# Kernel optimization log

Hardware: AMD Instinct MI355X
Metric: run time of the kernel (lower is better)

## Reference

```python
import jax, jax.numpy as jnp
import numpy as np

N_NODES = 100000
N_EDGES = 1600000
N_GRAPHS = 128


def _gru(x, w_ih, w_hh, b_ih, b_hh):
    # x: [N, T, D]; torch nn.GRU single layer, batch_first
    N, T, D = x.shape
    H = w_hh.shape[1]
    gi = jnp.einsum('ntd,gd->ntg', x, w_ih) + b_ih  # [N, T, 3H]

    def step(h, g_t):
        gh = h @ w_hh.T + b_hh
        i_r, i_z, i_n = jnp.split(g_t, 3, axis=-1)
        h_r, h_z, h_n = jnp.split(gh, 3, axis=-1)
        r = jax.nn.sigmoid(i_r + h_r)
        z = jax.nn.sigmoid(i_z + h_z)
        n = jnp.tanh(i_n + r * h_n)
        h_new = (1 - z) * n + z * h
        return h_new, None

    h0 = jnp.zeros((N, H), x.dtype)
    h, _ = jax.lax.scan(step, h0, jnp.swapaxes(gi, 0, 1))
    return h  # [N, H]


def _gat(x, W, att_src, att_dst, bias, src, dst, num_nodes, concat):
    # PyG GATConv: linear, per-head attention logits, segment softmax over dst, scatter-add
    H, C = att_src.shape
    xs = (x @ W).reshape(num_nodes, H, C)
    a_src = (xs * att_src).sum(-1)  # [N, H]
    a_dst = (xs * att_dst).sum(-1)  # [N, H]
    e = jax.nn.leaky_relu(a_src[src] + a_dst[dst], 0.2)  # [E, H]
    emax = jax.ops.segment_max(e, dst, num_segments=num_nodes)
    ee = jnp.exp(e - emax[dst])
    denom = jax.ops.segment_sum(ee, dst, num_segments=num_nodes)
    alpha = ee / (denom[dst] + 1e-16)
    msg = xs[src] * alpha[:, :, None]  # [E, H, C]
    out = jax.ops.segment_sum(msg, dst, num_segments=num_nodes)  # [N, H, C]
    if concat:
        out = out.reshape(num_nodes, H * C)
    else:
        out = out.mean(axis=1)
    return out + bias


def setup_inputs() -> dict:
    key = jax.random.key(0)
    ks = jax.random.split(key, 20)
    s = 0.05
    inp = {
        'x': jax.random.normal(ks[0], (N_NODES, 8, 128), jnp.float32),
        'edge_index': jax.random.randint(ks[1], (2, N_EDGES), 0, N_NODES, jnp.int32),
        'batch': jnp.sort(jax.random.randint(ks[2], (N_NODES,), 0, N_GRAPHS, jnp.int32)),
        'num_graphs': N_GRAPHS,
        'gru_w_ih': jax.random.normal(ks[3], (192, 128)) * s,
        'gru_w_hh': jax.random.normal(ks[4], (192, 64)) * s,
        'gru_b_ih': jax.random.normal(ks[5], (192,)) * s,
        'gru_b_hh': jax.random.normal(ks[6], (192,)) * s,
        'W1': jax.random.normal(ks[7], (64, 256)) * s,
        'att_src1': jax.random.normal(ks[8], (4, 64)) * s,
        'att_dst1': jax.random.normal(ks[9], (4, 64)) * s,
        'b1': jax.random.normal(ks[10], (256,)) * s,
        'W2': jax.random.normal(ks[11], (256, 64)) * s,
        'att_src2': jax.random.normal(ks[12], (1, 64)) * s,
        'att_dst2': jax.random.normal(ks[13], (1, 64)) * s,
        'b2': jax.random.normal(ks[14], (64,)) * s,
        'attn_w': jax.random.normal(ks[15], (64, 1)) * s,
        'attn_b': jax.random.normal(ks[16], (1,)) * s,
        'fc_w': jax.random.normal(ks[17], (64, 10)) * s,
        'fc_b': jax.random.normal(ks[18], (10,)) * s,
    }
    return inp


def reference(x, edge_index, batch, num_graphs, gru_w_ih, gru_w_hh, gru_b_ih, gru_b_hh,
              W1, att_src1, att_dst1, b1, W2, att_src2, att_dst2, b2,
              attn_w, attn_b, fc_w, fc_b):
    N = x.shape[0]
    h = _gru(x, gru_w_ih, gru_w_hh, gru_b_ih, gru_b_hh)  # [N, 64]
    # GATConv default add_self_loops=True
    loops = jnp.arange(N, dtype=edge_index.dtype)
    src = jnp.concatenate([edge_index[0], loops])
    dst = jnp.concatenate([edge_index[1], loops])
    h = jax.nn.relu(_gat(h, W1, att_src1, att_dst1, b1, src, dst, N, concat=True))   # [N, 256]
    h = jax.nn.relu(_gat(h, W2, att_src2, att_dst2, b2, src, dst, N, concat=False))  # [N, 64]
    # softmax over dim=1 of [N,1] -> all ones (faithful to the original code)
    aw = jax.nn.softmax(h @ attn_w + attn_b, axis=1)  # [N, 1]
    weighted = aw * h
    sums = jax.ops.segment_sum(weighted, batch, num_segments=num_graphs)  # [G, 64]
    counts = jax.ops.segment_sum(jnp.ones((N,), h.dtype), batch, num_segments=num_graphs)
    graph_feat = sums / jnp.maximum(counts, 1.0)[:, None]
    out = graph_feat @ fc_w + fc_b
    return jax.nn.log_softmax(out, axis=-1)
```

## Files before the change

kernel.cpp:

```cpp
#include <hip/hip_runtime.h>
#include <stdint.h>


typedef __attribute__((ext_vector_type(8))) short short8;
typedef __attribute__((ext_vector_type(4))) float f32x4;
typedef __attribute__((ext_vector_type(2))) float f32x2;
typedef __attribute__((ext_vector_type(2))) unsigned int u32x2;
typedef __attribute__((ext_vector_type(4))) unsigned int u32x4;

__device__ __forceinline__ unsigned short f2bf(float f) {
    unsigned u = __float_as_uint(f);
    u += 0x7FFFu + ((u >> 16) & 1u);
    return (unsigned short)(u >> 16);
}
__device__ __forceinline__ unsigned cvtpk(float lo, float hi) {
    unsigned r;
    asm("v_cvt_pk_bf16_f32 %0, %1, %2" : "=v"(r) : "v"(lo), "v"(hi));
    return r;
}
__device__ __forceinline__ unsigned short f2bfq(float v) {
    unsigned r;
    asm("v_cvt_pk_bf16_f32 %0, %1, %1" : "=v"(r) : "v"(v));
    return (unsigned short)r;
}
__device__ __forceinline__ float lrelu(float x) { return x > 0.f ? x : 0.2f * x; }
__device__ __forceinline__ float fsig(float a) {
    return __builtin_amdgcn_rcpf(1.f + __expf(-a));
}
__device__ __forceinline__ float ftanh(float a) {
    return 2.f * __builtin_amdgcn_rcpf(1.f + __expf(-2.f * a)) - 1.f;
}
__device__ __forceinline__ unsigned enc4fp8(float a, float b, float c, float d) {
    unsigned r = __builtin_amdgcn_cvt_pk_fp8_f32(a, b, 0, false);
    r = __builtin_amdgcn_cvt_pk_fp8_f32(c, d, r, true);
    return r;
}
__device__ __forceinline__ unsigned char enc1fp8(float v) {
    return (unsigned char)(__builtin_amdgcn_cvt_pk_fp8_f32(v, v, 0, false) & 0xff);
}

__device__ void pack_body(const float* __restrict__ src, unsigned short* __restrict__ dst,
                          int K, int NCOL, int ldsrc, int transposed, int blk, int tid) {
    int id = blk * 256 + tid;
    int KT = K >> 5;
    int nfrag = (NCOL >> 4) * KT;
    if (id >= nfrag * 64) return;
    int l = id & 63;
    int f = id >> 6;
    int kt = f % KT, ct = f / KT;
    int col = ct * 16 + (l & 15);
    int kbase = kt * 32 + ((l >> 4) << 3);
#pragma unroll
    for (int i = 0; i < 8; i++) {
        int k = kbase + i;
        float v = transposed ? src[(size_t)col * ldsrc + k] : src[(size_t)k * ldsrc + col];
        dst[((size_t)f * 64 + l) * 8 + i] = f2bf(v);
    }
}
__device__ void packv_body(const float* __restrict__ W, const float* __restrict__ avs,
                           const float* __restrict__ avd, unsigned short* __restrict__ dst,
                           int K, int H, int ldW, int blk, int tid) {
    int id = blk * 256 + tid;
    int KT = K >> 5;
    if (id >= KT * 64) return;
    int l = id & 63, f = id >> 6;
    int col = l & 15;
    int kbase = f * 32 + ((l >> 4) << 3);
    for (int i = 0; i < 8; i++) {
        int k = kbase + i;
        float val = 0.f;
        if (col < 2 * H) {
            int h = col >> 1;
            const float* av = (col & 1) ? avd : avs;
            for (int c = 0; c < 64; c++) val += W[(size_t)k * ldW + h * 64 + c] * av[h * 64 + c];
        }
        dst[((size_t)f * 64 + l) * 8 + i] = f2bf(val);
    }
}
__global__ void k_prep(const float* w_ih, const float* w_hh, const float* W1, const float* W2,
                       const float* as1, const float* ad1, const float* as2, const float* ad2,
                       const float* b1,
                       unsigned short* p_gi, unsigned short* p_gh,
                       unsigned short* p_w1, unsigned short* p_w2,
                       unsigned short* p_v1, unsigned short* p_v2,
                       float* b1p, int* cursor, int N) {
    int b = blockIdx.x, tid = threadIdx.x;
    if (b >= 38) {
        int i = (b - 38) * 256 + tid;
        if (i < N) cursor[i] = 0;
        return;
    }
    if (b < 12)      pack_body(w_ih, p_gi, 128, 192, 128, 1, b, tid);
    else if (b < 18) pack_body(w_hh, p_gh, 64, 192, 64, 1, b - 12, tid);
    else if (b < 26) pack_body(W1, p_w1, 64, 256, 256, 0, b - 18, tid);
    else if (b < 34) pack_body(W2, p_w2, 256, 64, 64, 0, b - 26, tid);
    else if (b < 35) packv_body(W1, as1, ad1, p_v1, 64, 4, 256, b - 34, tid);
    else if (b < 37) packv_body(W2, as2, ad2, p_v2, 256, 1, 64, b - 35, tid);
    else {
        int o = tid;
        int p = (o & 0xC0) | ((o & 15) << 2) | ((o >> 4) & 3);
        b1p[p] = b1[o];
    }
}

__launch_bounds__(256, 2)
__global__ void k_gru_gemm1(const float* __restrict__ x,
                            const unsigned short* __restrict__ pgi,
                            const unsigned short* __restrict__ pgh,
                            const float* __restrict__ b_ih, const float* __restrict__ b_hh,
                            const unsigned short* __restrict__ packB,
                            const unsigned short* __restrict__ pv1,
                            unsigned char* __restrict__ Cf,
                            float* __restrict__ aS, float* __restrict__ aD, int N) {
    __shared__ unsigned short x_pack[4 * 4 * 64 * 8];
    __shared__ unsigned short h_pack[4 * 2 * 64 * 8];

    const int tid = threadIdx.x;
    const int w = tid >> 6;
    const int l = tid & 63;
    const int row0 = blockIdx.x * 64;

    short8 wgi[3][4], wgh[3][2];
#pragma unroll
    for (int g = 0; g < 3; g++) {
        int ctg = g * 4 + w;
#pragma unroll
        for (int kt = 0; kt < 4; kt++)
            wgi[g][kt] = *(const short8*)(pgi + ((size_t)(ctg * 4 + kt) * 64 + l) * 8);
#pragma unroll
        for (int kt = 0; kt < 2; kt++)
            wgh[g][kt] = *(const short8*)(pgh + ((size_t)(ctg * 2 + kt) * 64 + l) * 8);
    }
    const int j = (w << 4) + (l & 15);
    const float bs_r = b_ih[j] + b_hh[j];
    const float bs_z = b_ih[64 + j] + b_hh[64 + j];
    const float bi_n = b_ih[128 + j], bh_n = b_hh[128 + j];

    f32x4 hreg[4];
    const f32x4 z4 = {0.f, 0.f, 0.f, 0.f};
#pragma unroll
    for (int m = 0; m < 4; m++) hreg[m] = z4;

    const int sr = tid >> 2, sub = tid & 3;
    const int snode = min(row0 + sr, N - 1);
    const int slane = (sr & 15) | (sub << 4);
    const int sm = sr >> 4;
    const float* xbase = x + (size_t)snode * 1024;

    float4 pre[8];
#pragma unroll
    for (int it = 0; it < 4; it++) {
        int d0 = it * 32 + sub * 8;
        pre[2 * it] = *(const float4*)(xbase + d0);
        pre[2 * it + 1] = *(const float4*)(xbase + d0 + 4);
    }

    for (int t = 0; t < 8; t++) {
        u32x4 pk[4];
#pragma unroll
        for (int it = 0; it < 4; it++) {
            float4 va = pre[2 * it], vb = pre[2 * it + 1];
            u32x4 p;
            p[0] = cvtpk(va.x, va.y); p[1] = cvtpk(va.z, va.w);
            p[2] = cvtpk(vb.x, vb.y); p[3] = cvtpk(vb.z, vb.w);
            pk[it] = p;
        }
        if (t > 0) {
#pragma unroll
            for (int m = 0; m < 4; m++)
#pragma unroll
                for (int q = 0; q < 4; q++) {
                    int rl = ((l >> 4) << 2) + q;
                    int lane2 = rl | (((j >> 3) & 3) << 4);
                    h_pack[((m * 2 + (j >> 5)) * 64 + lane2) * 8 + (j & 7)] = f2bfq(hreg[m][q]);
                }
        }
#pragma unroll
        for (int it = 0; it < 4; it++)
            *(u32x4*)&x_pack[((sm * 4 + it) * 64 + slane) * 8] = pk[it];
        __syncthreads();

        if (t < 7) {
            const float* xp = xbase + (t + 1) * 128;
#pragma unroll
            for (int it = 0; it < 4; it++) {
                int d0 = it * 32 + sub * 8;
                pre[2 * it] = *(const float4*)(xp + d0);
                pre[2 * it + 1] = *(const float4*)(xp + d0 + 4);
            }
        }

        f32x4 agi[4][3], aghn[4];
#pragma unroll
        for (int m = 0; m < 4; m++) {
            agi[m][0] = z4; agi[m][1] = z4; agi[m][2] = z4; aghn[m] = z4;
        }

#pragma unroll
        for (int m = 0; m < 4; m++) {
#pragma unroll
            for (int kt = 0; kt < 4; kt++) {
                short8 a = *(const short8*)&x_pack[((m * 4 + kt) * 64 + l) * 8];
#pragma unroll
                for (int g = 0; g < 3; g++)
                    agi[m][g] = __builtin_amdgcn_mfma_f32_16x16x32_bf16(a, wgi[g][kt], agi[m][g], 0, 0, 0);
            }
            if (t > 0) {
#pragma unroll
                for (int kt = 0; kt < 2; kt++) {
                    short8 a = *(const short8*)&h_pack[((m * 2 + kt) * 64 + l) * 8];
                    agi[m][0] = __builtin_amdgcn_mfma_f32_16x16x32_bf16(a, wgh[0][kt], agi[m][0], 0, 0, 0);
                    agi[m][1] = __builtin_amdgcn_mfma_f32_16x16x32_bf16(a, wgh[1][kt], agi[m][1], 0, 0, 0);
                    aghn[m]   = __builtin_amdgcn_mfma_f32_16x16x32_bf16(a, wgh[2][kt], aghn[m], 0, 0, 0);
                }
            }
        }
#pragma unroll
        for (int m = 0; m < 4; m++) {
#pragma unroll
            for (int q = 0; q < 4; q++) {
                float rr = fsig(agi[m][0][q] + bs_r);
                float zz = fsig(agi[m][1][q] + bs_z);
                float hn = aghn[m][q] + bh_n;
                float nn = ftanh(agi[m][2][q] + bi_n + rr * hn);
                hreg[m][q] = nn + zz * (hreg[m][q] - nn);
            }
        }
        __syncthreads();
    }

    short8 bfw[4][2];
#pragma unroll
    for (int ci = 0; ci < 4; ci++)
#pragma unroll
        for (int kt = 0; kt < 2; kt++)
            bfw[ci][kt] = *(const short8*)(packB + ((size_t)((w * 4 + ci) * 2 + kt) * 64 + l) * 8);
    short8 bev[2];
#pragma unroll
    for (int kt = 0; kt < 2; kt++)
        bev[kt] = *(const short8*)(pv1 + ((size_t)kt * 64 + l) * 8);

#pragma unroll
    for (int m = 0; m < 4; m++)
#pragma unroll
        for (int q = 0; q < 4; q++) {
            int rl = ((l >> 4) << 2) + q;
            int lane2 = rl | (((j >> 3) & 3) << 4);
            h_pack[((m * 2 + (j >> 5)) * 64 + lane2) * 8 + (j & 7)] = f2bfq(hreg[m][q]);
        }
    __syncthreads();

    f32x4 acc[4][4];
#pragma unroll
    for (int m = 0; m < 4; m++)
#pragma unroll
        for (int ci = 0; ci < 4; ci++) acc[m][ci] = z4;

#pragma unroll
    for (int m = 0; m < 4; m++)
#pragma unroll
        for (int kt = 0; kt < 2; kt++) {
            short8 a = *(const short8*)&h_pack[((m * 2 + kt) * 64 + l) * 8];
#pragma unroll
            for (int ci = 0; ci < 4; ci++)
                acc[m][ci] = __builtin_amdgcn_mfma_f32_16x16x32_bf16(a, bfw[ci][kt], acc[m][ci], 0, 0, 0);
        }

    f32x4 acce = z4;
#pragma unroll
    for (int kt = 0; kt < 2; kt++) {
        short8 a = *(const short8*)&h_pack[((w * 2 + kt) * 64 + l) * 8];
        acce = __builtin_amdgcn_mfma_f32_16x16x32_bf16(a, bev[kt], acce, 0, 0, 0);
    }
    int colE = l & 15;
    if (colE < 8) {
        int h = colE >> 1;
#pragma unroll
        for (int q = 0; q < 4; q++) {
            int node = row0 + (w << 4) + ((l >> 4) << 2) + q;
            if (node < N) {
                if (colE & 1) aD[node * 4 + h] = acce[q];
                else          aS[node * 4 + h] = acce[q];
            }
        }
    }
    const int lc = l & 15;
#pragma unroll
    for (int m = 0; m < 4; m++)
#pragma unroll
        for (int q = 0; q < 4; q++) {
            int node = row0 + (m << 4) + ((l >> 4) << 2) + q;
            if (node < N) {
                unsigned d = enc4fp8(acc[m][0][q], acc[m][1][q], acc[m][2][q], acc[m][3][q]);
                *(unsigned*)(Cf + (size_t)node * 256 + w * 64 + lc * 4) = d;
            }
        }
}

__global__ void k_fill(const int* __restrict__ srcv, const int* __restrict__ dstv,
                       int* __restrict__ cursor, int* __restrict__ ssrc, int E) {
    int i = blockIdx.x * blockDim.x + threadIdx.x;
    if (i < E) {
        int d = dstv[i];
        int pos = atomicAdd(&cursor[d], 1);
        if (pos < 64) ssrc[(size_t)d * 64 + pos] = srcv[i];
    }
}

__global__ void k_agg1(const unsigned char* __restrict__ xs,
                       const float* __restrict__ a_s, const float* __restrict__ a_d,
                       const int* __restrict__ deg, const int* __restrict__ ssrc,
                       const float* __restrict__ b1p,
                       unsigned short* __restrict__ h2, int N) {
    const int v = blockIdx.x * 16 + (threadIdx.x >> 4);
    if (v >= N) return;
    const int cq = threadIdx.x & 15;
    const int H = cq >> 2;
    const float adv = a_d[v * 4 + H];
    const int cnt = min(deg[v], 64);
    const size_t base = (size_t)v * 64;

    float s_;
    float ac[16];
    {
        u32x4 xv = *(const u32x4*)(xs + (size_t)v * 256 + cq * 16);
        float pv = __expf(lrelu(a_s[v * 4 + H] + adv));
        s_ = pv;
#pragma unroll
        for (int wd = 0; wd < 4; wd++) {
            f32x2 lo = __builtin_amdgcn_cvt_pk_f32_fp8(xv[wd], false);
            f32x2 hi = __builtin_amdgcn_cvt_pk_f32_fp8(xv[wd], true);
            ac[wd * 4 + 0] = pv * lo[0]; ac[wd * 4 + 1] = pv * lo[1];
            ac[wd * 4 + 2] = pv * hi[0]; ac[wd * 4 + 3] = pv * hi[1];
        }
    }

#define AG1_LOAD(S, POS) { int pp = min((POS), cl); int uu = ssrc[base + pp]; \
        aa##S = a_s[uu * 4 + H]; x##S = *(const u32x4*)(xs + (size_t)uu * 256 + cq * 16); }
#define AG1_PROC(S, PRED) { float p = (PRED) ? __expf(lrelu(aa##S + adv)) : 0.f; s_ += p; \
        _Pragma("unroll") for (int wd = 0; wd < 4; wd++) { \
            f32x2 lo = __builtin_amdgcn_cvt_pk_f32_fp8(x##S[wd], false); \
            f32x2 hi = __builtin_amdgcn_cvt_pk_f32_fp8(x##S[wd], true); \
            ac[wd * 4 + 0] += p * lo[0]; ac[wd * 4 + 1] += p * lo[1]; \
            ac[wd * 4 + 2] += p * hi[0]; ac[wd * 4 + 3] += p * hi[1]; } }

    float aa0 = 0.f, aa1 = 0.f, aa2 = 0.f, aa3 = 0.f;
    u32x4 x0 = {0,0,0,0}, x1 = {0,0,0,0}, x2 = {0,0,0,0}, x3 = {0,0,0,0};
    if (cnt > 0) {
        const int cl = cnt - 1;
        AG1_LOAD(0, 0) AG1_LOAD(1, 1) AG1_LOAD(2, 2) AG1_LOAD(3, 3)
        int k = 0;
        for (; k + 4 <= cnt; k += 4) {
            AG1_PROC(0, true) AG1_LOAD(0, k + 4)
            AG1_PROC(1, true) AG1_LOAD(1, k + 5)
            AG1_PROC(2, true) AG1_LOAD(2, k + 6)
            AG1_PROC(3, true) AG1_LOAD(3, k + 7)
        }
        AG1_PROC(0, k + 0 < cnt)
        AG1_PROC(1, k + 1 < cnt)
        AG1_PROC(2, k + 2 < cnt)
        AG1_PROC(3, k + 3 < cnt)
    }
#undef AG1_LOAD
#undef AG1_PROC

    float inv = __builtin_amdgcn_rcpf(s_ + 1e-16f);
    float bp[16];
#pragma unroll
    for (int i = 0; i < 4; i++)
        *(float4*)&bp[i * 4] = *(const float4*)(b1p + cq * 16 + i * 4);
#pragma unroll
    for (int b = 0; b < 4; b++) {
        float r0 = fmaxf(ac[b]      * inv + bp[b],      0.f);
        float r1 = fmaxf(ac[4 + b]  * inv + bp[4 + b],  0.f);
        float r2 = fmaxf(ac[8 + b]  * inv + bp[8 + b],  0.f);
        float r3 = fmaxf(ac[12 + b] * inv + bp[12 + b], 0.f);
        u32x2 o;
        o[0] = cvtpk(r0, r1); o[1] = cvtpk(r2, r3);
        *(u32x2*)(h2 + (size_t)v * 256 + H * 64 + b * 16 + (cq & 3) * 4) = o;
    }
}

__launch_bounds__(256, 2)
__global__ void k_gemm2(const unsigned short* __restrict__ A,
                        const unsigned short* __restrict__ packB,
                        const unsigned short* __restrict__ pv2,
                        unsigned char* __restrict__ Cf,
                        float* __restrict__ aS, float* __restrict__ aD, int N) {
    constexpr int KT = 8;
    __shared__ unsigned short a_pack[4 * KT * 64 * 8];

    const int tid = threadIdx.x, w = tid >> 6, l = tid & 63;
    const int row0 = blockIdx.x * 64;

    short8 bf[KT];
#pragma unroll
    for (int kt = 0; kt < KT; kt++)
        bf[kt] = *(const short8*)(packB + ((size_t)(w * KT + kt) * 64 + l) * 8);

    const int sr = tid >> 2, sub = tid & 3;
    const int snode = min(row0 + sr, N - 1);
    const unsigned short* ap = A + (size_t)snode * 256;
#pragma unroll
    for (int it = 0; it < KT; it++) {
        int d0 = it * 32 + sub * 8;
        short8 v = *(const short8*)(ap + d0);
        *(short8*)&a_pack[(((sr >> 4) * KT + it) * 64 + ((sr & 15) | (sub << 4))) * 8] = v;
    }
    __syncthreads();

    const f32x4 z4 = {0.f, 0.f, 0.f, 0.f};
    f32x4 acc[4];
#pragma unroll
    for (int m = 0; m < 4; m++) acc[m] = z4;

#pragma unroll
    for (int m = 0; m < 4; m++)
#pragma unroll
        for (int kt = 0; kt < KT; kt++) {
            short8 a = *(const short8*)&a_pack[((m * KT + kt) * 64 + l) * 8];
            acc[m] = __builtin_amdgcn_mfma_f32_16x16x32_bf16(a, bf[kt], acc[m], 0, 0, 0);
        }

    f32x4 acce = z4;
#pragma unroll
    for (int kt = 0; kt < KT; kt++) {
        short8 be = *(const short8*)(pv2 + ((size_t)kt * 64 + l) * 8);
        short8 a = *(const short8*)&a_pack[((w * KT + kt) * 64 + l) * 8];
        acce = __builtin_amdgcn_mfma_f32_16x16x32_bf16(a, be, acce, 0, 0, 0);
    }
    int colE = l & 15;
    if (colE < 2) {
#pragma unroll
        for (int q = 0; q < 4; q++) {
            int node = row0 + (w << 4) + ((l >> 4) << 2) + q;
            if (node < N) {
                if (colE) aD[node] = acce[q];
                else      aS[node] = acce[q];
            }
        }
    }

    int colw = w * 16 + (l & 15);
#pragma unroll
    for (int m = 0; m < 4; m++)
#pragma unroll
        for (int q = 0; q < 4; q++) {
            int node = row0 + (m << 4) + ((l >> 4) << 2) + q;
            if (node < N) Cf[(size_t)node * 64 + colw] = enc1fp8(acc[m][q]);
        }
}

__global__ void k_agg2(const unsigned char* __restrict__ xs,
                       const float* __restrict__ a_s, const float* __restrict__ a_d,
                       const int* __restrict__ deg, const int* __restrict__ ssrc,
                       const float* __restrict__ bias,
                       float* __restrict__ out, int N) {
    const int v = blockIdx.x * 32 + (threadIdx.x >> 3);
    if (v >= N) return;
    const int cq = threadIdx.x & 7;
    const int c0 = cq * 8;
    const float adv = a_d[v];
    const int cnt = min(deg[v], 64);
    const size_t base = (size_t)v * 64;

    float s_;
    float ac[8];
    {
        u32x2 xv = *(const u32x2*)(xs + (size_t)v * 64 + c0);
        float pv = __expf(lrelu(a_s[v] + adv));
        s_ = pv;
#pragma unroll
        for (int wd = 0; wd < 2; wd++) {
            f32x2 lo = __builtin_amdgcn_cvt_pk_f32_fp8(xv[wd], false);
            f32x2 hi = __builtin_amdgcn_cvt_pk_f32_fp8(xv[wd], true);
            ac[wd * 4 + 0] = pv * lo[0]; ac[wd * 4 + 1] = pv * lo[1];
            ac[wd * 4 + 2] = pv * hi[0]; ac[wd * 4 + 3] = pv * hi[1];
        }
    }

#define AG2_LOAD(S, POS) { int pp = min((POS), cl); int uu = ssrc[base + pp]; \
        aa##S = a_s[uu]; x##S = *(const u32x2*)(xs + (size_t)uu * 64 + c0); }
#define AG2_PROC(S, PRED) { float p = (PRED) ? __expf(lrelu(aa##S + adv)) : 0.f; s_ += p; \
        _Pragma("unroll") for (int wd = 0; wd < 2; wd++) { \
            f32x2 lo = __builtin_amdgcn_cvt_pk_f32_fp8(x##S[wd], false); \
            f32x2 hi = __builtin_amdgcn_cvt_pk_f32_fp8(x##S[wd], true); \
            ac[wd * 4 + 0] += p * lo[0]; ac[wd * 4 + 1] += p * lo[1]; \
            ac[wd * 4 + 2] += p * hi[0]; ac[wd * 4 + 3] += p * hi[1]; } }

    float aa0 = 0.f, aa1 = 0.f, aa2 = 0.f, aa3 = 0.f;
    u32x2 x0 = {0,0}, x1 = {0,0}, x2 = {0,0}, x3 = {0,0};
    if (cnt > 0) {
        const int cl = cnt - 1;
        AG2_LOAD(0, 0) AG2_LOAD(1, 1) AG2_LOAD(2, 2) AG2_LOAD(3, 3)
        int k = 0;
        for (; k + 4 <= cnt; k += 4) {
            AG2_PROC(0, true) AG2_LOAD(0, k + 4)
            AG2_PROC(1, true) AG2_LOAD(1, k + 5)
            AG2_PROC(2, true) AG2_LOAD(2, k + 6)
            AG2_PROC(3, true) AG2_LOAD(3, k + 7)
        }
        AG2_PROC(0, k + 0 < cnt)
        AG2_PROC(1, k + 1 < cnt)
        AG2_PROC(2, k + 2 < cnt)
        AG2_PROC(3, k + 3 < cnt)
    }
#undef AG2_LOAD
#undef AG2_PROC

    float inv = __builtin_amdgcn_rcpf(s_ + 1e-16f);
    float4 b4a = *(const float4*)(bias + c0);
    float4 b4b = *(const float4*)(bias + c0 + 4);
    float4 o1, o2;
    o1.x = fmaxf(ac[0] * inv + b4a.x, 0.f);
    o1.y = fmaxf(ac[1] * inv + b4a.y, 0.f);
    o1.z = fmaxf(ac[2] * inv + b4a.z, 0.f);
    o1.w = fmaxf(ac[3] * inv + b4a.w, 0.f);
    o2.x = fmaxf(ac[4] * inv + b4b.x, 0.f);
    o2.y = fmaxf(ac[5] * inv + b4b.y, 0.f);
    o2.z = fmaxf(ac[6] * inv + b4b.z, 0.f);
    o2.w = fmaxf(ac[7] * inv + b4b.w, 0.f);
    *(float4*)(out + (size_t)v * 64 + c0) = o1;
    *(float4*)(out + (size_t)v * 64 + c0 + 4) = o2;
}

__global__ void k_pool(const float* __restrict__ h3, const int* __restrict__ batch,
                       const float* __restrict__ fc_w, const float* __restrict__ fc_b,
                       float* __restrict__ out, int N, int G) {
    __shared__ float red[4][64];
    __shared__ float meanv[64];
    __shared__ float lg[10];
    int g = blockIdx.x;
    int tid = threadIdx.x, c = tid & 63, ro = tid >> 6;
    int lo = 0, hi = N;
    while (lo < hi) { int mid = (lo + hi) >> 1; if (batch[mid] < g) lo = mid + 1; else hi = mid; }
    int s0 = lo;
    lo = 0; hi = N;
    while (lo < hi) { int mid = (lo + hi) >> 1; if (batch[mid] < g + 1) lo = mid + 1; else hi = mid; }
    int s1 = lo;
    float p = 0.f;
    for (int r = s0 + ro; r < s1; r += 4) p += h3[(size_t)r * 64 + c];
    red[ro][c] = p;
    __syncthreads();
    if (tid < 64) {
        float tot = red[0][c] + red[1][c] + red[2][c] + red[3][c];
        float cnt = (float)max(s1 - s0, 1);
        meanv[c] = tot / cnt;
    }
    __syncthreads();
    if (tid < 10) {
        float lv = fc_b[tid];
        for (int k = 0; k < 64; k++) lv += meanv[k] * fc_w[k * 10 + tid];
        lg[tid] = lv;
    }
    __syncthreads();
    if (tid == 0) {
        float mxv = lg[0];
        for (int k = 1; k < 10; k++) mxv = fmaxf(mxv, lg[k]);
        float ss = 0.f;
        for (int k = 0; k < 10; k++) ss += expf(lg[k] - mxv);
        float lse = mxv + logf(ss);
        for (int k = 0; k < 10; k++) out[g * 10 + k] = lg[k] - lse;
    }
}

extern "C" void kernel_launch(void* const* d_in, const int* in_sizes, int n_in,
                              void* d_out, int out_size, void* d_ws, size_t ws_size,
                              hipStream_t stream) {
    const float* x = (const float*)d_in[0];
    const int* ei = (const int*)d_in[1];
    const int* batch = (const int*)d_in[2];
    const float* w_ih = (const float*)d_in[4];
    const float* w_hh = (const float*)d_in[5];
    const float* b_ih = (const float*)d_in[6];
    const float* b_hh = (const float*)d_in[7];
    const float* W1 = (const float*)d_in[8];
    const float* as1 = (const float*)d_in[9];
    const float* ad1 = (const float*)d_in[10];
    const float* b1 = (const float*)d_in[11];
    const float* W2 = (const float*)d_in[12];
    const float* as2 = (const float*)d_in[13];
    const float* ad2 = (const float*)d_in[14];
    const float* b2 = (const float*)d_in[15];
    const float* fc_w = (const float*)d_in[18];
    const float* fc_b = (const float*)d_in[19];
    float* out = (float*)d_out;

    const int N = in_sizes[0] / (8 * 128);
    const int E = in_sizes[1] / 2;
    const int G = 128;

    char* ws = (char*)d_ws;
    size_t cur = 0;
    auto alloc = [&](size_t b) { size_t r = cur; cur += (b + 255) & ~(size_t)255; return r; };
    unsigned short* p_gi = (unsigned short*)(ws + alloc((size_t)12 * 4 * 64 * 8 * 2));
    unsigned short* p_gh = (unsigned short*)(ws + alloc((size_t)12 * 2 * 64 * 8 * 2));
    unsigned short* p_w1 = (unsigned short*)(ws + alloc((size_t)16 * 2 * 64 * 8 * 2));
    unsigned short* p_w2 = (unsigned short*)(ws + alloc((size_t)4 * 8 * 64 * 8 * 2));
    unsigned short* p_v1 = (unsigned short*)(ws + alloc((size_t)2 * 64 * 8 * 2));
    unsigned short* p_v2 = (unsigned short*)(ws + alloc((size_t)8 * 64 * 8 * 2));
    float* b1p = (float*)(ws + alloc((size_t)256 * 4));
    unsigned char* xs1f = (unsigned char*)(ws + alloc((size_t)N * 256));
    unsigned char* xs2f = (unsigned char*)(ws + alloc((size_t)N * 64));
    unsigned short* h2 = (unsigned short*)(ws + alloc((size_t)N * 256 * 2));
    float* h3 = (float*)(ws + alloc((size_t)N * 64 * 4));
    float* aS = (float*)(ws + alloc((size_t)N * 4 * 4));
    float* aD = (float*)(ws + alloc((size_t)N * 4 * 4));
    float* aS2 = (float*)(ws + alloc((size_t)N * 4));
    float* aD2 = (float*)(ws + alloc((size_t)N * 4));
    int* cursor = (int*)(ws + alloc((size_t)N * 4));
    int* ssrc = (int*)(ws + alloc((size_t)N * 64 * 4));

    const int nb64 = (N + 63) / 64;

    k_prep<<<38 + (N + 255) / 256, 256, 0, stream>>>(
        w_ih, w_hh, W1, W2, as1, ad1, as2, ad2, b1,
        p_gi, p_gh, p_w1, p_w2, p_v1, p_v2, b1p, cursor, N);

    k_fill<<<(E + 255) / 256, 256, 0, stream>>>(ei, ei + E, cursor, ssrc, E);

    k_gru_gemm1<<<nb64, 256, 0, stream>>>(x, p_gi, p_gh, b_ih, b_hh,
                                          p_w1, p_v1, xs1f, aS, aD, N);

    k_agg1<<<(N + 15) / 16, 256, 0, stream>>>(xs1f, aS, aD, cursor, ssrc, b1p, h2, N);

    k_gemm2<<<nb64, 256, 0, stream>>>(h2, p_w2, p_v2, xs2f, aS2, aD2, N);

    k_agg2<<<(N + 31) / 32, 256, 0, stream>>>(xs2f, aS2, aD2, cursor, ssrc, b2, h3, N);

    k_pool<<<G, 256, 0, stream>>>(h3, batch, fc_w, fc_b, out, N, G);
}
```

Before: 420.8 us.

## Double-buffer GRU LDS tiles and deepen gather prefetch in GAT aggregation

The GRU kernel now ping-pongs x_pack and h_pack between two LDS buffers. The next timestep's packed input and hidden state are written after the gate math, so each step needs only one barrier instead of two, and global loads of x run two steps ahead. Both GAT aggregation kernels raise the software-pipelined neighbour gather depth from 4 to 8 in-flight loads and issue them before the self-loop term. This is meant to hide more gather latency. In exchange it raises register pressure and doubles the LDS use of the GRU kernel, which could lower occupancy.

```diff
diff --git a/kernel.cpp b/kernel.cpp
--- a/kernel.cpp
+++ b/kernel.cpp
@@ -112,8 +112,8 @@
                             const unsigned short* __restrict__ pv1,
                             unsigned char* __restrict__ Cf,
                             float* __restrict__ aS, float* __restrict__ aD, int N) {
-    __shared__ unsigned short x_pack[4 * 4 * 64 * 8];
-    __shared__ unsigned short h_pack[4 * 2 * 64 * 8];
+    __shared__ unsigned short x_pack[2][4 * 4 * 64 * 8];
+    __shared__ unsigned short h_pack[2][4 * 2 * 64 * 8];
 
     const int tid = threadIdx.x;
     const int w = tid >> 6;
@@ -154,53 +154,35 @@
         pre[2 * it] = *(const float4*)(xbase + d0);
         pre[2 * it + 1] = *(const float4*)(xbase + d0 + 4);
     }
+#pragma unroll
+    for (int it = 0; it < 4; it++) {
+        float4 va = pre[2 * it], vb = pre[2 * it + 1];
+        u32x4 p;
+        p[0] = cvtpk(va.x, va.y); p[1] = cvtpk(va.z, va.w);
+        p[2] = cvtpk(vb.x, vb.y); p[3] = cvtpk(vb.z, vb.w);
+        *(u32x4*)&x_pack[0][((sm * 4 + it) * 64 + slane) * 8] = p;
+    }
+#pragma unroll
+    for (int it = 0; it < 4; it++) {
+        int d0 = it * 32 + sub * 8;
+        pre[2 * it] = *(const float4*)(xbase + 128 + d0);
+        pre[2 * it + 1] = *(const float4*)(xbase + 128 + d0 + 4);
+    }
+    __syncthreads();
 
     for (int t = 0; t < 8; t++) {
-        u32x4 pk[4];
-#pragma unroll
-        for (int it = 0; it < 4; it++) {
-            float4 va = pre[2 * it], vb = pre[2 * it + 1];
-            u32x4 p;
-            p[0] = cvtpk(va.x, va.y); p[1] = cvtpk(va.z, va.w);
-            p[2] = cvtpk(vb.x, vb.y); p[3] = cvtpk(vb.z, vb.w);
-            pk[it] = p;
-        }
-        if (t > 0) {
-#pragma unroll
-            for (int m = 0; m < 4; m++)
-#pragma unroll
-                for (int q = 0; q < 4; q++) {
-                    int rl = ((l >> 4) << 2) + q;
-                    int lane2 = rl | (((j >> 3) & 3) << 4);
-                    h_pack[((m * 2 + (j >> 5)) * 64 + lane2) * 8 + (j & 7)] = f2bfq(hreg[m][q]);
-                }
-        }
-#pragma unroll
-        for (int it = 0; it < 4; it++)
-            *(u32x4*)&x_pack[((sm * 4 + it) * 64 + slane) * 8] = pk[it];
-        __syncthreads();
-
-        if (t < 7) {
-            const float* xp = xbase + (t + 1) * 128;
-#pragma unroll
-            for (int it = 0; it < 4; it++) {
-                int d0 = it * 32 + sub * 8;
-                pre[2 * it] = *(const float4*)(xp + d0);
-                pre[2 * it + 1] = *(const float4*)(xp + d0 + 4);
-            }
-        }
+        const int p = t & 1;
 
         f32x4 agi[4][3], aghn[4];
 #pragma unroll
         for (int m = 0; m < 4; m++) {
             agi[m][0] = z4; agi[m][1] = z4; agi[m][2] = z4; aghn[m] = z4;
         }
-
 #pragma unroll
         for (int m = 0; m < 4; m++) {
 #pragma unroll
             for (int kt = 0; kt < 4; kt++) {
-                short8 a = *(const short8*)&x_pack[((m * 4 + kt) * 64 + l) * 8];
+                short8 a = *(const short8*)&x_pack[p][((m * 4 + kt) * 64 + l) * 8];
 #pragma unroll
                 for (int g = 0; g < 3; g++)
                     agi[m][g] = __builtin_amdgcn_mfma_f32_16x16x32_bf16(a, wgi[g][kt], agi[m][g], 0, 0, 0);
@@ -208,7 +190,7 @@
             if (t > 0) {
 #pragma unroll
                 for (int kt = 0; kt < 2; kt++) {
-                    short8 a = *(const short8*)&h_pack[((m * 2 + kt) * 64 + l) * 8];
+                    short8 a = *(const short8*)&h_pack[p][((m * 2 + kt) * 64 + l) * 8];
                     agi[m][0] = __builtin_amdgcn_mfma_f32_16x16x32_bf16(a, wgh[0][kt], agi[m][0], 0, 0, 0);
                     agi[m][1] = __builtin_amdgcn_mfma_f32_16x16x32_bf16(a, wgh[1][kt], agi[m][1], 0, 0, 0);
                     aghn[m]   = __builtin_amdgcn_mfma_f32_16x16x32_bf16(a, wgh[2][kt], aghn[m], 0, 0, 0);
@@ -226,6 +208,38 @@
                 hreg[m][q] = nn + zz * (hreg[m][q] - nn);
             }
         }
+
+        if (t < 7) {
+            u32x4 pk[4];
+#pragma unroll
+            for (int it = 0; it < 4; it++) {
+                float4 va = pre[2 * it], vb = pre[2 * it + 1];
+                u32x4 pp;
+                pp[0] = cvtpk(va.x, va.y); pp[1] = cvtpk(va.z, va.w);
+                pp[2] = cvtpk(vb.x, vb.y); pp[3] = cvtpk(vb.z, vb.w);
+                pk[it] = pp;
+            }
+            if (t < 6) {
+                const float* xp = xbase + (t + 2) * 128;
+#pragma unroll
+                for (int it = 0; it < 4; it++) {
+                    int d0 = it * 32 + sub * 8;
+                    pre[2 * it] = *(const float4*)(xp + d0);
+                    pre[2 * it + 1] = *(const float4*)(xp + d0 + 4);
+                }
+            }
+#pragma unroll
+            for (int it = 0; it < 4; it++)
+                *(u32x4*)&x_pack[p ^ 1][((sm * 4 + it) * 64 + slane) * 8] = pk[it];
+#pragma unroll
+            for (int m = 0; m < 4; m++)
+#pragma unroll
+                for (int q = 0; q < 4; q++) {
+                    int rl = ((l >> 4) << 2) + q;
+                    int lane2 = rl | (((j >> 3) & 3) << 4);
+                    h_pack[p ^ 1][((m * 2 + (j >> 5)) * 64 + lane2) * 8 + (j & 7)] = f2bfq(hreg[m][q]);
+                }
+        }
         __syncthreads();
     }
 
@@ -246,7 +260,7 @@
         for (int q = 0; q < 4; q++) {
             int rl = ((l >> 4) << 2) + q;
             int lane2 = rl | (((j >> 3) & 3) << 4);
-            h_pack[((m * 2 + (j >> 5)) * 64 + lane2) * 8 + (j & 7)] = f2bfq(hreg[m][q]);
+            h_pack[0][((m * 2 + (j >> 5)) * 64 + lane2) * 8 + (j & 7)] = f2bfq(hreg[m][q]);
         }
     __syncthreads();
 
@@ -260,7 +274,7 @@
     for (int m = 0; m < 4; m++)
 #pragma unroll
         for (int kt = 0; kt < 2; kt++) {
-            short8 a = *(const short8*)&h_pack[((m * 2 + kt) * 64 + l) * 8];
+            short8 a = *(const short8*)&h_pack[0][((m * 2 + kt) * 64 + l) * 8];
 #pragma unroll
             for (int ci = 0; ci < 4; ci++)
                 acc[m][ci] = __builtin_amdgcn_mfma_f32_16x16x32_bf16(a, bfw[ci][kt], acc[m][ci], 0, 0, 0);
@@ -269,7 +283,7 @@
     f32x4 acce = z4;
 #pragma unroll
     for (int kt = 0; kt < 2; kt++) {
-        short8 a = *(const short8*)&h_pack[((w * 2 + kt) * 64 + l) * 8];
+        short8 a = *(const short8*)&h_pack[0][((w * 2 + kt) * 64 + l) * 8];
         acce = __builtin_amdgcn_mfma_f32_16x16x32_bf16(a, bev[kt], acce, 0, 0, 0);
     }
     int colE = l & 15;
@@ -320,21 +334,6 @@
     const int cnt = min(deg[v], 64);
     const size_t base = (size_t)v * 64;
 
-    float s_;
-    float ac[16];
-    {
-        u32x4 xv = *(const u32x4*)(xs + (size_t)v * 256 + cq * 16);
-        float pv = __expf(lrelu(a_s[v * 4 + H] + adv));
-        s_ = pv;
-#pragma unroll
-        for (int wd = 0; wd < 4; wd++) {
-            f32x2 lo = __builtin_amdgcn_cvt_pk_f32_fp8(xv[wd], false);
-            f32x2 hi = __builtin_amdgcn_cvt_pk_f32_fp8(xv[wd], true);
-            ac[wd * 4 + 0] = pv * lo[0]; ac[wd * 4 + 1] = pv * lo[1];
-            ac[wd * 4 + 2] = pv * hi[0]; ac[wd * 4 + 3] = pv * hi[1];
-        }
-    }
-
 #define AG1_LOAD(S, POS) { int pp = min((POS), cl); int uu = ssrc[base + pp]; \
         aa##S = a_s[uu * 4 + H]; x##S = *(const u32x4*)(xs + (size_t)uu * 256 + cq * 16); }
 #define AG1_PROC(S, PRED) { float p = (PRED) ? __expf(lrelu(aa##S + adv)) : 0.f; s_ += p; \
@@ -345,21 +344,50 @@
             ac[wd * 4 + 2] += p * hi[0]; ac[wd * 4 + 3] += p * hi[1]; } }
 
     float aa0 = 0.f, aa1 = 0.f, aa2 = 0.f, aa3 = 0.f;
+    float aa4 = 0.f, aa5 = 0.f, aa6 = 0.f, aa7 = 0.f;
     u32x4 x0 = {0,0,0,0}, x1 = {0,0,0,0}, x2 = {0,0,0,0}, x3 = {0,0,0,0};
+    u32x4 x4 = {0,0,0,0}, x5 = {0,0,0,0}, x6 = {0,0,0,0}, x7 = {0,0,0,0};
+    const int cl = (cnt > 0) ? (cnt - 1) : 0;
     if (cnt > 0) {
-        const int cl = cnt - 1;
         AG1_LOAD(0, 0) AG1_LOAD(1, 1) AG1_LOAD(2, 2) AG1_LOAD(3, 3)
+        AG1_LOAD(4, 4) AG1_LOAD(5, 5) AG1_LOAD(6, 6) AG1_LOAD(7, 7)
+    }
+
+    float s_;
+    float ac[16];
+    {
+        u32x4 xv = *(const u32x4*)(xs + (size_t)v * 256 + cq * 16);
+        float pv = __expf(lrelu(a_s[v * 4 + H] + adv));
+        s_ = pv;
+#pragma unroll
+        for (int wd = 0; wd < 4; wd++) {
+            f32x2 lo = __builtin_amdgcn_cvt_pk_f32_fp8(xv[wd], false);
+            f32x2 hi = __builtin_amdgcn_cvt_pk_f32_fp8(xv[wd], true);
+            ac[wd * 4 + 0] = pv * lo[0]; ac[wd * 4 + 1] = pv * lo[1];
+            ac[wd * 4 + 2] = pv * hi[0]; ac[wd * 4 + 3] = pv * hi[1];
+        }
+    }
+
+    if (cnt > 0) {
         int k = 0;
-        for (; k + 4 <= cnt; k += 4) {
-            AG1_PROC(0, true) AG1_LOAD(0, k + 4)
-            AG1_PROC(1, true) AG1_LOAD(1, k + 5)
-            AG1_PROC(2, true) AG1_LOAD(2, k + 6)
-            AG1_PROC(3, true) AG1_LOAD(3, k + 7)
+        for (; k + 8 <= cnt; k += 8) {
+            AG1_PROC(0, true) AG1_LOAD(0, k + 8)
+            AG1_PROC(1, true) AG1_LOAD(1, k + 9)
+            AG1_PROC(2, true) AG1_LOAD(2, k + 10)
+            AG1_PROC(3, true) AG1_LOAD(3, k + 11)
+            AG1_PROC(4, true) AG1_LOAD(4, k + 12)
+            AG1_PROC(5, true) AG1_LOAD(5, k + 13)
+            AG1_PROC(6, true) AG1_LOAD(6, k + 14)
+            AG1_PROC(7, true) AG1_LOAD(7, k + 15)
         }
         AG1_PROC(0, k + 0 < cnt)
         AG1_PROC(1, k + 1 < cnt)
         AG1_PROC(2, k + 2 < cnt)
         AG1_PROC(3, k + 3 < cnt)
+        AG1_PROC(4, k + 4 < cnt)
+        AG1_PROC(5, k + 5 < cnt)
+        AG1_PROC(6, k + 6 < cnt)
+        AG1_PROC(7, k + 7 < cnt)
     }
 #undef AG1_LOAD
 #undef AG1_PROC
@@ -464,21 +492,6 @@
     const int cnt = min(deg[v], 64);
     const size_t base = (size_t)v * 64;
 
-    float s_;
-    float ac[8];
-    {
-        u32x2 xv = *(const u32x2*)(xs + (size_t)v * 64 + c0);
-        float pv = __expf(lrelu(a_s[v] + adv));
-        s_ = pv;
-#pragma unroll
-        for (int wd = 0; wd < 2; wd++) {
-            f32x2 lo = __builtin_amdgcn_cvt_pk_f32_fp8(xv[wd], false);
-            f32x2 hi = __builtin_amdgcn_cvt_pk_f32_fp8(xv[wd], true);
-            ac[wd * 4 + 0] = pv * lo[0]; ac[wd * 4 + 1] = pv * lo[1];
-            ac[wd * 4 + 2] = pv * hi[0]; ac[wd * 4 + 3] = pv * hi[1];
-        }
-    }
-
 #define AG2_LOAD(S, POS) { int pp = min((POS), cl); int uu = ssrc[base + pp]; \
         aa##S = a_s[uu]; x##S = *(const u32x2*)(xs + (size_t)uu * 64 + c0); }
 #define AG2_PROC(S, PRED) { float p = (PRED) ? __expf(lrelu(aa##S + adv)) : 0.f; s_ += p; \
@@ -489,21 +502,50 @@
             ac[wd * 4 + 2] += p * hi[0]; ac[wd * 4 + 3] += p * hi[1]; } }
 
     float aa0 = 0.f, aa1 = 0.f, aa2 = 0.f, aa3 = 0.f;
+    float aa4 = 0.f, aa5 = 0.f, aa6 = 0.f, aa7 = 0.f;
     u32x2 x0 = {0,0}, x1 = {0,0}, x2 = {0,0}, x3 = {0,0};
+    u32x2 x4 = {0,0}, x5 = {0,0}, x6 = {0,0}, x7 = {0,0};
+    const int cl = (cnt > 0) ? (cnt - 1) : 0;
     if (cnt > 0) {
-        const int cl = cnt - 1;
         AG2_LOAD(0, 0) AG2_LOAD(1, 1) AG2_LOAD(2, 2) AG2_LOAD(3, 3)
+        AG2_LOAD(4, 4) AG2_LOAD(5, 5) AG2_LOAD(6, 6) AG2_LOAD(7, 7)
+    }
+
+    float s_;
+    float ac[8];
+    {
+        u32x2 xv = *(const u32x2*)(xs + (size_t)v * 64 + c0);
+        float pv = __expf(lrelu(a_s[v] + adv));
+        s_ = pv;
+#pragma unroll
+        for (int wd = 0; wd < 2; wd++) {
+            f32x2 lo = __builtin_amdgcn_cvt_pk_f32_fp8(xv[wd], false);
+            f32x2 hi = __builtin_amdgcn_cvt_pk_f32_fp8(xv[wd], true);
+            ac[wd * 4 + 0] = pv * lo[0]; ac[wd * 4 + 1] = pv * lo[1];
+            ac[wd * 4 + 2] = pv * hi[0]; ac[wd * 4 + 3] = pv * hi[1];
+        }
+    }
+
+    if (cnt > 0) {
         int k = 0;
-        for (; k + 4 <= cnt; k += 4) {
-            AG2_PROC(0, true) AG2_LOAD(0, k + 4)
-            AG2_PROC(1, true) AG2_LOAD(1, k + 5)
-            AG2_PROC(2, true) AG2_LOAD(2, k + 6)
-            AG2_PROC(3, true) AG2_LOAD(3, k + 7)
+        for (; k + 8 <= cnt; k += 8) {
+            AG2_PROC(0, true) AG2_LOAD(0, k + 8)
+            AG2_PROC(1, true) AG2_LOAD(1, k + 9)
+            AG2_PROC(2, true) AG2_LOAD(2, k + 10)
+            AG2_PROC(3, true) AG2_LOAD(3, k + 11)
+            AG2_PROC(4, true) AG2_LOAD(4, k + 12)
+            AG2_PROC(5, true) AG2_LOAD(5, k + 13)
+            AG2_PROC(6, true) AG2_LOAD(6, k + 14)
+            AG2_PROC(7, true) AG2_LOAD(7, k + 15)
         }
         AG2_PROC(0, k + 0 < cnt)
         AG2_PROC(1, k + 1 < cnt)
         AG2_PROC(2, k + 2 < cnt)
         AG2_PROC(3, k + 3 < cnt)
+        AG2_PROC(4, k + 4 < cnt)
+        AG2_PROC(5, k + 5 < cnt)
+        AG2_PROC(6, k + 6 < cnt)
+        AG2_PROC(7, k + 7 < cnt)
     }
 #undef AG2_LOAD
 #undef AG2_PROC
```

Measured after the change: 499.3 us. 18.7% more time.
